# Kernel tuning notes

Hardware: AMD Instinct MI355X
Metric: run time of the kernel (lower is better)

Reference implementation:

```python
import jax, jax.numpy as jnp
import numpy as np

S, H, T = 65536, 768, 6   # seq_len, hidden, n_types
K, WIN = 3, 15            # top-k starts, end-pointer window
TYPE_THRESH, START_THRESH = 0.3, 0.15


def setup_inputs() -> dict:
    key = jax.random.key(0)
    ks = jax.random.split(key, 9)
    sc = 0.02
    return {
        "token_embeds": jax.random.normal(ks[0], (S, H), dtype=jnp.float32),
        "W_start": jax.random.normal(ks[1], (H, T), dtype=jnp.float32) * sc,
        "b_start": jnp.zeros((T,), dtype=jnp.float32),
        "W_end": jax.random.normal(ks[2], (H, T), dtype=jnp.float32) * sc,
        "b_end": jnp.zeros((T,), dtype=jnp.float32),
        "W1": jax.random.normal(ks[3], (H, 64), dtype=jnp.float32) * sc,
        "b1": jnp.zeros((64,), dtype=jnp.float32),
        "W2": jax.random.normal(ks[4], (64, T), dtype=jnp.float32) * sc,
        "b2": jnp.zeros((T,), dtype=jnp.float32),
    }


def reference(token_embeds, W_start, b_start, W_end, b_end, W1, b1, W2, b2):
    # Pointer projections: (S, T)
    start_scores = token_embeds @ W_start + b_start
    end_scores = token_embeds @ W_end + b_end

    # Type confidence head on mean-pooled embedding (torch nn.GELU = exact erf)
    pooled = token_embeds.mean(axis=0)                      # (H,)
    h = jax.nn.gelu(pooled @ W1 + b1, approximate=False)    # (64,)
    type_conf = jax.nn.sigmoid(h @ W2 + b2)                 # (T,)

    # Softmax over sequence dim per type, then top-3 candidate starts per type
    s_probs = jax.nn.softmax(start_scores, axis=0)          # (S, T)
    top_vals, top_idx = jax.lax.top_k(s_probs.T, K)         # (T, K)

    # Windowed argmax over end_scores[s : s+15, t]
    pos = top_idx[:, :, None] + jnp.arange(WIN)
    in_range = pos < S
    pos_c = jnp.clip(pos, 0, S - 1)
    end_T = end_scores.T                                    # (T, S)
    window_vals = end_T[jnp.arange(T)[:, None, None], pos_c]
    window_vals = jnp.where(in_range, window_vals, -jnp.inf)
    e_off = jnp.argmax(window_vals, axis=-1)                # (T, K)

    starts = top_idx                                        # (T, K) int
    ends = top_idx + e_off + 1                              # exclusive end, matches e+1
    valid = (type_conf[:, None] >= TYPE_THRESH) & (top_vals >= START_THRESH)
    conf = jnp.where(valid, top_vals * type_conf[:, None], 0.0)  # (T, K)

    return conf, starts, ends, valid
```

## Files before the change

### kernel.cpp

```cpp
#include <hip/hip_runtime.h>
#include <math.h>

#define S_TOK 65536
#define H_DIM 768
#define T_TYPES 6
#define K_TOP 3
#define WIN 15
#define NBLK1 512
#define NWAVES (NBLK1 * 4)
#define ROWS_PER_WAVE (S_TOK / NWAVES)
#define POOL_CHUNKS 8
#define BLK_PER_CHUNK (NBLK1 / POOL_CHUNKS)

__device__ __forceinline__ void top3_insert(float v, int i,
    float& v0, float& v1, float& v2, int& i0, int& i1, int& i2)
{
    if (v > v0 || (v == v0 && i < i0)) {
        v2 = v1; i2 = i1; v1 = v0; i1 = i0; v0 = v; i0 = i;
    } else if (v > v1 || (v == v1 && i < i1)) {
        v2 = v1; i2 = i1; v1 = v; i1 = i;
    } else if (v > v2 || (v == v2 && i < i2)) {
        v2 = v; i2 = i;
    }
}

__device__ __forceinline__ void merge_state(
    float& M, float& se, float& v0, float& v1, float& v2,
    int& i0, int& i1, int& i2,
    float Mb, float seb, float w0, float w1, float w2,
    int j0, int j1, int j2)
{
    const float Mn = fmaxf(M, Mb);
    se = se * expf(M - Mn) + seb * expf(Mb - Mn);
    M = Mn;
    top3_insert(w0, j0, v0, v1, v2, i0, i1, i2);
    top3_insert(w1, j1, v0, v1, v2, i0, i1, i2);
    top3_insert(w2, j2, v0, v1, v2, i0, i1, i2);
}

__global__ __launch_bounds__(256, 2) void k_scores(
    const float* __restrict__ emb,
    const float* __restrict__ Wstart, const float* __restrict__ bstart,
    const float* __restrict__ Wend,   const float* __restrict__ bend,
    float* __restrict__ endS,
    float* __restrict__ partials,
    float* __restrict__ pooledPart)
{
    const int lane = threadIdx.x & 63;
    const int wib  = threadIdx.x >> 6;
    const int wave = blockIdx.x * 4 + wib;

    const bool b5 = (lane & 32) != 0;
    const bool b4 = (lane & 16) != 0;
    const bool b3 = (lane & 8)  != 0;
    const bool b2 = (lane & 4)  != 0;
    const int  sem = (b5 ? 6 : 0) + (b4 ? 3 : 0) + (b3 ? 2 : (b2 ? 1 : 0));
    const bool desig   = ((lane & 3) == 0) && !(b3 && b2);
    const bool isStart = desig && !b5;
    const bool isEnd   = desig && b5;

    float wS[3][4][T_TYPES], wE[3][4][T_TYPES];
#pragma unroll
    for (int j = 0; j < 3; ++j)
#pragma unroll
        for (int c = 0; c < 4; ++c) {
            const int h = 4 * (lane + 64 * j) + c;
#pragma unroll
            for (int t = 0; t < T_TYPES; ++t) {
                wS[j][c][t] = Wstart[h * T_TYPES + t];
                wE[j][c][t] = Wend  [h * T_TYPES + t];
            }
        }

    float myBias = 0.0f;
    if (isStart) myBias = bstart[sem];
    if (isEnd)   myBias = bend[sem - T_TYPES];

    float pool[3][4] = {};

    float M  = -3.402823466e38f, se = 0.0f;
    float v0 = -3.402823466e38f, v1 = v0, v2 = v0;
    int   i0 = -1, i1 = -1, i2 = -1;

    const int r0 = wave * ROWS_PER_WAVE;
    const float4* rowp = (const float4*)emb + (size_t)r0 * (H_DIM / 4);
    float4 c0 = rowp[lane], c1 = rowp[lane + 64], c2 = rowp[lane + 128];

    for (int r = r0; r < r0 + ROWS_PER_WAVE; ++r) {
        const float4* nextp = rowp + ((r + 1 < S_TOK) ? (H_DIM / 4) : 0);
        float4 n0 = nextp[lane], n1 = nextp[lane + 64], n2 = nextp[lane + 128];

        float acc[12];
#pragma unroll
        for (int a = 0; a < 12; ++a) acc[a] = 0.0f;

        const float4 ee[3] = {c0, c1, c2};
#pragma unroll
        for (int j = 0; j < 3; ++j) {
            const float ev[4] = {ee[j].x, ee[j].y, ee[j].z, ee[j].w};
#pragma unroll
            for (int c = 0; c < 4; ++c) {
                const float v = ev[c];
                pool[j][c] += v;
#pragma unroll
                for (int t = 0; t < T_TYPES; ++t) {
                    acc[t]           = fmaf(v, wS[j][c][t], acc[t]);
                    acc[T_TYPES + t] = fmaf(v, wE[j][c][t], acc[T_TYPES + t]);
                }
            }
        }

        float na[6];
#pragma unroll
        for (int t = 0; t < 6; ++t) {
            const float snd  = b5 ? acc[t] : acc[t + 6];
            const float keep = b5 ? acc[t + 6] : acc[t];
            na[t] = keep + __shfl_xor(snd, 32, 64);
        }
        float nb[3];
#pragma unroll
        for (int t = 0; t < 3; ++t) {
            const float snd  = b4 ? na[t] : na[t + 3];
            const float keep = b4 ? na[t + 3] : na[t];
            nb[t] = keep + __shfl_xor(snd, 16, 64);
        }
        float nc0, nc1;
        {
            const float snd  = b3 ? nb[2] : nb[0];
            const float keep = b3 ? nb[2] : nb[0];
            nc0 = keep + __shfl_xor(b3 ? nb[0] : nb[2], 8, 64);
            (void)snd;
            nc1 = nb[1] + __shfl_xor(nb[1], 8, 64);
        }
        float d;
        {
            const float snd  = (b3 || b2) ? nc0 : nc1;
            const float keep = (!b3 && b2) ? nc1 : nc0;
            d = keep + __shfl_xor(snd, 4, 64);
        }
        d += __shfl_xor(d, 2, 64);
        d += __shfl_xor(d, 1, 64);

        const float v = d + myBias;

        if (isStart) {
            if (v > M) {
                se = se * expf(M - v) + 1.0f;
                v2 = v1; i2 = i1; v1 = v0; i1 = i0; v0 = v; i0 = r;
                M = v;
            } else {
                se += expf(v - M);
                if (v > v2 || (v == v2 && r < i2)) {
                    if (v > v1 || (v == v1 && r < i1)) {
                        v2 = v1; i2 = i1; v1 = v; i1 = r;
                    } else { v2 = v; i2 = r; }
                }
            }
        } else if (isEnd) {
            endS[(size_t)(sem - T_TYPES) * S_TOK + r] = v;
        }

        c0 = n0; c1 = n1; c2 = n2; rowp = nextp;
    }

    if (isStart) {
        float* p = partials + ((size_t)wave * T_TYPES + sem) * 8;
        p[0] = M;  p[1] = se; p[2] = v0; p[3] = v1; p[4] = v2;
        p[5] = __int_as_float(i0);
        p[6] = __int_as_float(i1);
        p[7] = __int_as_float(i2);
    }

    __shared__ float lds[4][H_DIM];
#pragma unroll
    for (int j = 0; j < 3; ++j) {
        float4 pv = make_float4(pool[j][0], pool[j][1], pool[j][2], pool[j][3]);
        ((float4*)lds[wib])[lane + 64 * j] = pv;
    }
    __syncthreads();
    for (int h = threadIdx.x; h < H_DIM; h += 256) {
        pooledPart[(size_t)blockIdx.x * H_DIM + h] =
            (lds[0][h] + lds[1][h]) + (lds[2][h] + lds[3][h]);
    }
}

__global__ __launch_bounds__(1024) void k_mid(
    const float* __restrict__ partials,
    const float* __restrict__ pooledPart,
    const float* __restrict__ W1,
    float* __restrict__ zpart,
    float* __restrict__ res)
{
    const int b = blockIdx.x;
    const int tid = threadIdx.x;

    if (b >= T_TYPES) {
        const int c = b - T_TYPES;
        __shared__ float pl[H_DIM];
        if (tid < H_DIM) {
            const float* base = pooledPart + (size_t)c * BLK_PER_CHUNK * H_DIM + tid;
            float s0 = 0, s1 = 0, s2 = 0, s3 = 0;
            for (int i = 0; i < BLK_PER_CHUNK; i += 4) {
                s0 += base[(size_t)(i + 0) * H_DIM];
                s1 += base[(size_t)(i + 1) * H_DIM];
                s2 += base[(size_t)(i + 2) * H_DIM];
                s3 += base[(size_t)(i + 3) * H_DIM];
            }
            pl[tid] = (s0 + s1) + (s2 + s3);
        }
        __syncthreads();
        const int o = tid & 63, seg = tid >> 6;
        float z = 0.0f;
        const int h0 = seg * 48;
        for (int i = 0; i < 48; ++i)
            z = fmaf(pl[h0 + i], W1[(size_t)(h0 + i) * 64 + o], z);
        __shared__ float zred[16][64];
        zred[seg][o] = z;
        __syncthreads();
        if (tid < 64) {
            float s = 0.0f;
#pragma unroll
            for (int g = 0; g < 16; ++g) s += zred[g][tid];
            zpart[c * 64 + tid] = s;
        }
        return;
    }

    float M, se, v0, v1, v2; int i0, i1, i2;
    {
        const float* p = partials + ((size_t)tid * T_TYPES + b) * 8;
        M = p[0]; se = p[1]; v0 = p[2]; v1 = p[3]; v2 = p[4];
        i0 = __float_as_int(p[5]); i1 = __float_as_int(p[6]); i2 = __float_as_int(p[7]);
    }
    {
        const float* p = partials + ((size_t)(tid + 1024) * T_TYPES + b) * 8;
        merge_state(M, se, v0, v1, v2, i0, i1, i2,
                    p[0], p[1], p[2], p[3], p[4],
                    __float_as_int(p[5]), __float_as_int(p[6]), __float_as_int(p[7]));
    }

#pragma unroll
    for (int msk = 1; msk < 64; msk <<= 1) {
        const float Mb  = __shfl_xor(M,  msk, 64);
        const float seb = __shfl_xor(se, msk, 64);
        const float w0  = __shfl_xor(v0, msk, 64);
        const float w1  = __shfl_xor(v1, msk, 64);
        const float w2  = __shfl_xor(v2, msk, 64);
        const int   j0  = __shfl_xor(i0, msk, 64);
        const int   j1  = __shfl_xor(i1, msk, 64);
        const int   j2  = __shfl_xor(i2, msk, 64);
        merge_state(M, se, v0, v1, v2, i0, i1, i2, Mb, seb, w0, w1, w2, j0, j1, j2);
    }

    __shared__ float sm[16][8];
    if ((tid & 63) == 0) {
        const int w = tid >> 6;
        sm[w][0] = M;  sm[w][1] = se;
        sm[w][2] = v0; sm[w][3] = v1; sm[w][4] = v2;
        sm[w][5] = __int_as_float(i0);
        sm[w][6] = __int_as_float(i1);
        sm[w][7] = __int_as_float(i2);
    }
    __syncthreads();
    if (tid == 0) {
        for (int w = 1; w < 16; ++w) {
            merge_state(M, se, v0, v1, v2, i0, i1, i2,
                        sm[w][0], sm[w][1], sm[w][2], sm[w][3], sm[w][4],
                        __float_as_int(sm[w][5]), __float_as_int(sm[w][6]),
                        __float_as_int(sm[w][7]));
        }
        float* r = res + b * 8;
        r[0] = v0; r[1] = v1; r[2] = v2;
        r[3] = __int_as_float(i0);
        r[4] = __int_as_float(i1);
        r[5] = __int_as_float(i2);
        r[6] = M; r[7] = se;
    }
}

__global__ __launch_bounds__(256) void k_final(
    const float* __restrict__ zpart,
    const float* __restrict__ b1,
    const float* __restrict__ W2, const float* __restrict__ b2,
    const float* __restrict__ endS, const float* __restrict__ res,
    float* __restrict__ out)
{
    const int tid = threadIdx.x;
    __shared__ float hdn[64];
    if (tid < 64) {
        float zs = 0.0f;
#pragma unroll
        for (int c = 0; c < POOL_CHUNKS; ++c) zs += zpart[c * 64 + tid];
        const float z = zs * (1.0f / (float)S_TOK) + b1[tid];
        hdn[tid] = 0.5f * z * (1.0f + erff(z * 0.7071067811865475f));
    }
    __syncthreads();

    __shared__ float tconf[T_TYPES];
    if (tid < T_TYPES) {
        float z = b2[tid];
        for (int i = 0; i < 64; ++i) z = fmaf(hdn[i], W2[i * T_TYPES + tid], z);
        tconf[tid] = 1.0f / (1.0f + expf(-z));
    }
    __syncthreads();

    if (tid < T_TYPES * K_TOP) {
        const int t = tid / K_TOP;
        const int k = tid % K_TOP;
        const float* r = res + t * 8;
        const float vraw = r[k];
        const int   idx  = __float_as_int(r[3 + k]);
        const float M    = r[6];
        const float SE   = r[7];
        const float prob = expf(vraw - M) / SE;

        const float* ecol = endS + (size_t)t * S_TOK;
        float best = -3.402823466e38f;
        int   boff = 0;
#pragma unroll
        for (int w = 0; w < WIN; ++w) {
            const int pos = idx + w;
            if (pos < S_TOK) {
                const float ev = ecol[pos];
                if (ev > best) { best = ev; boff = w; }
            }
        }
        const float tc = tconf[t];
        const bool valid = (tc >= 0.3f) && (prob >= 0.15f);
        out[tid]      = valid ? prob * tc : 0.0f;
        out[18 + tid] = (float)idx;
        out[36 + tid] = (float)(idx + boff + 1);
        out[54 + tid] = valid ? 1.0f : 0.0f;
    }
}

extern "C" void kernel_launch(void* const* d_in, const int* in_sizes, int n_in,
                              void* d_out, int out_size, void* d_ws, size_t ws_size,
                              hipStream_t stream)
{
    const float* emb    = (const float*)d_in[0];
    const float* Wstart = (const float*)d_in[1];
    const float* bstart = (const float*)d_in[2];
    const float* Wend   = (const float*)d_in[3];
    const float* bend   = (const float*)d_in[4];
    const float* W1     = (const float*)d_in[5];
    const float* b1     = (const float*)d_in[6];
    const float* W2     = (const float*)d_in[7];
    const float* b2     = (const float*)d_in[8];
    float* out = (float*)d_out;

    float* ws       = (float*)d_ws;
    float* endS     = ws;
    float* partials = endS + (size_t)T_TYPES * S_TOK;
    float* pp       = partials + (size_t)NWAVES * T_TYPES * 8;
    float* zpart    = pp + (size_t)NBLK1 * H_DIM;
    float* res      = zpart + (size_t)POOL_CHUNKS * 64;

    k_scores<<<NBLK1, 256, 0, stream>>>(emb, Wstart, bstart, Wend, bend,
                                        endS, partials, pp);
    k_mid<<<T_TYPES + POOL_CHUNKS, 1024, 0, stream>>>(partials, pp, W1, zpart, res);
    k_final<<<1, 256, 0, stream>>>(zpart, b1, W2, b2, endS, res, out);
}
```

Baseline: 341.0 us.

## Split projection types across waves sharing rows to cut register pressure

Each block now owns a contiguous row range, and its four waves all read the same rows. Each wave computes three output columns: start or end, types 0-2 or 3-5. This cuts per-lane weight registers from 144 to 36 and simplifies the cross-lane shuffle reduction, which allows a higher occupancy bound of 4 blocks per CU and 2048 blocks. The cost is that each row is loaded by four waves, so the design relies on L1/L2 to absorb the redundant reads, and the number of pooled and start partials to merge downstream grows.

After: 349.3 us. 2.5% more time.

```diff
diff --git a/kernel.cpp b/kernel.cpp
--- a/kernel.cpp
+++ b/kernel.cpp
@@ -6,10 +6,10 @@
 #define T_TYPES 6
 #define K_TOP 3
 #define WIN 15
-#define NBLK1 512
-#define NWAVES (NBLK1 * 4)
-#define ROWS_PER_WAVE (S_TOK / NWAVES)
-#define POOL_CHUNKS 8
+#define NBLK1 2048
+#define ROWS_PER_BLK (S_TOK / NBLK1)
+#define NRANGES NBLK1
+#define POOL_CHUNKS 16
 #define BLK_PER_CHUNK (NBLK1 / POOL_CHUNKS)
 
 __device__ __forceinline__ void top3_insert(float v, int i,
@@ -38,7 +38,7 @@
     top3_insert(w2, j2, v0, v1, v2, i0, i1, i2);
 }
 
-__global__ __launch_bounds__(256, 2) void k_scores(
+__global__ __launch_bounds__(256, 4) void k_scores(
     const float* __restrict__ emb,
     const float* __restrict__ Wstart, const float* __restrict__ bstart,
     const float* __restrict__ Wend,   const float* __restrict__ bend,
@@ -48,139 +48,109 @@
 {
     const int lane = threadIdx.x & 63;
     const int wib  = threadIdx.x >> 6;
-    const int wave = blockIdx.x * 4 + wib;
-
+    const bool isStartW = (wib < 2);
+    const int  tbase = (wib & 1) * 3;
     const bool b5 = (lane & 32) != 0;
     const bool b4 = (lane & 16) != 0;
-    const bool b3 = (lane & 8)  != 0;
-    const bool b2 = (lane & 4)  != 0;
-    const int  sem = (b5 ? 6 : 0) + (b4 ? 3 : 0) + (b3 ? 2 : (b2 ? 1 : 0));
-    const bool desig   = ((lane & 3) == 0) && !(b3 && b2);
-    const bool isStart = desig && !b5;
-    const bool isEnd   = desig && b5;
-
-    float wS[3][4][T_TYPES], wE[3][4][T_TYPES];
+    const int  sem = b4 ? 2 : (b5 ? 1 : 0);
+    const bool desig = (lane == 0) || (lane == 16) || (lane == 32);
+
+    const float* Wmat = isStartW ? Wstart : Wend;
+    float wG[3][4][3];
 #pragma unroll
     for (int j = 0; j < 3; ++j)
 #pragma unroll
         for (int c = 0; c < 4; ++c) {
             const int h = 4 * (lane + 64 * j) + c;
 #pragma unroll
-            for (int t = 0; t < T_TYPES; ++t) {
-                wS[j][c][t] = Wstart[h * T_TYPES + t];
-                wE[j][c][t] = Wend  [h * T_TYPES + t];
-            }
+            for (int u = 0; u < 3; ++u)
+                wG[j][c][u] = Wmat[h * T_TYPES + tbase + u];
         }
 
     float myBias = 0.0f;
-    if (isStart) myBias = bstart[sem];
-    if (isEnd)   myBias = bend[sem - T_TYPES];
-
-    float pool[3][4] = {};
+    if (desig) myBias = (isStartW ? bstart : bend)[tbase + sem];
+
+    float4 pool[3];
+#pragma unroll
+    for (int j = 0; j < 3; ++j) pool[j] = make_float4(0.f, 0.f, 0.f, 0.f);
 
     float M  = -3.402823466e38f, se = 0.0f;
     float v0 = -3.402823466e38f, v1 = v0, v2 = v0;
     int   i0 = -1, i1 = -1, i2 = -1;
 
-    const int r0 = wave * ROWS_PER_WAVE;
+    const int r0 = blockIdx.x * ROWS_PER_BLK;
     const float4* rowp = (const float4*)emb + (size_t)r0 * (H_DIM / 4);
     float4 c0 = rowp[lane], c1 = rowp[lane + 64], c2 = rowp[lane + 128];
 
-    for (int r = r0; r < r0 + ROWS_PER_WAVE; ++r) {
+    for (int r = r0; r < r0 + ROWS_PER_BLK; ++r) {
         const float4* nextp = rowp + ((r + 1 < S_TOK) ? (H_DIM / 4) : 0);
         float4 n0 = nextp[lane], n1 = nextp[lane + 64], n2 = nextp[lane + 128];
 
-        float acc[12];
-#pragma unroll
-        for (int a = 0; a < 12; ++a) acc[a] = 0.0f;
-
+        float a0 = 0.0f, a1 = 0.0f, a2 = 0.0f;
         const float4 ee[3] = {c0, c1, c2};
 #pragma unroll
         for (int j = 0; j < 3; ++j) {
             const float ev[4] = {ee[j].x, ee[j].y, ee[j].z, ee[j].w};
+            pool[j].x += ev[0]; pool[j].y += ev[1];
+            pool[j].z += ev[2]; pool[j].w += ev[3];
 #pragma unroll
             for (int c = 0; c < 4; ++c) {
                 const float v = ev[c];
-                pool[j][c] += v;
-#pragma unroll
-                for (int t = 0; t < T_TYPES; ++t) {
-                    acc[t]           = fmaf(v, wS[j][c][t], acc[t]);
-                    acc[T_TYPES + t] = fmaf(v, wE[j][c][t], acc[T_TYPES + t]);
+                a0 = fmaf(v, wG[j][c][0], a0);
+                a1 = fmaf(v, wG[j][c][1], a1);
+                a2 = fmaf(v, wG[j][c][2], a2);
+            }
+        }
+
+        float snd = b5 ? a0 : a1;
+        float kp  = b5 ? a1 : a0;
+        float x0 = kp + __shfl_xor(snd, 32, 64);
+        float x1 = a2 + __shfl_xor(a2, 32, 64);
+        snd = b4 ? x0 : x1;
+        kp  = b4 ? x1 : x0;
+        float y = kp + __shfl_xor(snd, 16, 64);
+        y += __shfl_xor(y, 8, 64);
+        y += __shfl_xor(y, 4, 64);
+        y += __shfl_xor(y, 2, 64);
+        y += __shfl_xor(y, 1, 64);
+
+        const float v = y + myBias;
+
+        if (isStartW) {
+            if (desig) {
+                if (v > M) {
+                    se = se * expf(M - v) + 1.0f;
+                    v2 = v1; i2 = i1; v1 = v0; i1 = i0; v0 = v; i0 = r;
+                    M = v;
+                } else {
+                    se += expf(v - M);
+                    if (v > v2 || (v == v2 && r < i2)) {
+                        if (v > v1 || (v == v1 && r < i1)) {
+                            v2 = v1; i2 = i1; v1 = v; i1 = r;
+                        } else { v2 = v; i2 = r; }
+                    }
                 }
             }
-        }
-
-        float na[6];
-#pragma unroll
-        for (int t = 0; t < 6; ++t) {
-            const float snd  = b5 ? acc[t] : acc[t + 6];
-            const float keep = b5 ? acc[t + 6] : acc[t];
-            na[t] = keep + __shfl_xor(snd, 32, 64);
-        }
-        float nb[3];
-#pragma unroll
-        for (int t = 0; t < 3; ++t) {
-            const float snd  = b4 ? na[t] : na[t + 3];
-            const float keep = b4 ? na[t + 3] : na[t];
-            nb[t] = keep + __shfl_xor(snd, 16, 64);
-        }
-        float nc0, nc1;
-        {
-            const float snd  = b3 ? nb[2] : nb[0];
-            const float keep = b3 ? nb[2] : nb[0];
-            nc0 = keep + __shfl_xor(b3 ? nb[0] : nb[2], 8, 64);
-            (void)snd;
-            nc1 = nb[1] + __shfl_xor(nb[1], 8, 64);
-        }
-        float d;
-        {
-            const float snd  = (b3 || b2) ? nc0 : nc1;
-            const float keep = (!b3 && b2) ? nc1 : nc0;
-            d = keep + __shfl_xor(snd, 4, 64);
-        }
-        d += __shfl_xor(d, 2, 64);
-        d += __shfl_xor(d, 1, 64);
-
-        const float v = d + myBias;
-
-        if (isStart) {
-            if (v > M) {
-                se = se * expf(M - v) + 1.0f;
-                v2 = v1; i2 = i1; v1 = v0; i1 = i0; v0 = v; i0 = r;
-                M = v;
-            } else {
-                se += expf(v - M);
-                if (v > v2 || (v == v2 && r < i2)) {
-                    if (v > v1 || (v == v1 && r < i1)) {
-                        v2 = v1; i2 = i1; v1 = v; i1 = r;
-                    } else { v2 = v; i2 = r; }
-                }
-            }
-        } else if (isEnd) {
-            endS[(size_t)(sem - T_TYPES) * S_TOK + r] = v;
+        } else {
+            if (desig) endS[(size_t)(tbase + sem) * S_TOK + r] = v;
         }
 
         c0 = n0; c1 = n1; c2 = n2; rowp = nextp;
     }
 
-    if (isStart) {
-        float* p = partials + ((size_t)wave * T_TYPES + sem) * 8;
+    if (isStartW && desig) {
+        float* p = partials + ((size_t)blockIdx.x * T_TYPES + (tbase + sem)) * 8;
         p[0] = M;  p[1] = se; p[2] = v0; p[3] = v1; p[4] = v2;
         p[5] = __int_as_float(i0);
         p[6] = __int_as_float(i1);
         p[7] = __int_as_float(i2);
     }
 
-    __shared__ float lds[4][H_DIM];
-#pragma unroll
-    for (int j = 0; j < 3; ++j) {
-        float4 pv = make_float4(pool[j][0], pool[j][1], pool[j][2], pool[j][3]);
-        ((float4*)lds[wib])[lane + 64 * j] = pv;
-    }
-    __syncthreads();
-    for (int h = threadIdx.x; h < H_DIM; h += 256) {
-        pooledPart[(size_t)blockIdx.x * H_DIM + h] =
-            (lds[0][h] + lds[1][h]) + (lds[2][h] + lds[3][h]);
+    if (wib == 3) {
+        float4* pp4 = (float4*)(pooledPart + (size_t)blockIdx.x * H_DIM);
+        pp4[lane]       = pool[0];
+        pp4[lane + 64]  = pool[1];
+        pp4[lane + 128] = pool[2];
     }
 }
 
@@ -199,14 +169,14 @@
         __shared__ float pl[H_DIM];
         if (tid < H_DIM) {
             const float* base = pooledPart + (size_t)c * BLK_PER_CHUNK * H_DIM + tid;
-            float s0 = 0, s1 = 0, s2 = 0, s3 = 0;
-            for (int i = 0; i < BLK_PER_CHUNK; i += 4) {
-                s0 += base[(size_t)(i + 0) * H_DIM];
-                s1 += base[(size_t)(i + 1) * H_DIM];
-                s2 += base[(size_t)(i + 2) * H_DIM];
-                s3 += base[(size_t)(i + 3) * H_DIM];
+            float s[8] = {0, 0, 0, 0, 0, 0, 0, 0};
+            for (int i = 0; i < BLK_PER_CHUNK; i += 8) {
+#pragma unroll
+                for (int u = 0; u < 8; ++u)
+                    s[u] += base[(size_t)(i + u) * H_DIM];
             }
-            pl[tid] = (s0 + s1) + (s2 + s3);
+            pl[tid] = ((s[0] + s[1]) + (s[2] + s[3])) +
+                      ((s[4] + s[5]) + (s[6] + s[7]));
         }
         __syncthreads();
         const int o = tid & 63, seg = tid >> 6;
@@ -352,7 +322,7 @@
     float* ws       = (float*)d_ws;
     float* endS     = ws;
     float* partials = endS + (size_t)T_TYPES * S_TOK;
-    float* pp       = partials + (size_t)NWAVES * T_TYPES * 8;
+    float* pp       = partials + (size_t)NRANGES * T_TYPES * 8;
     float* zpart    = pp + (size_t)NBLK1 * H_DIM;
     float* res      = zpart + (size_t)POOL_CHUNKS * 64;
 
```

## Fuse final kernel into mid via last-block ticket; write per-wave pooled partials

Applied to the files above, without the earlier changes.

Removes the third kernel launch by having the last block of k_mid, chosen with an atomic ticket, compute the type-confidence head and the windowed end argmax. k_scores now writes per-wave pooled partials straight to global memory instead of reducing the four waves through LDS with a block barrier. POOL_CHUNKS is doubled so more blocks share the larger pooled reduction. The cost is a fourfold larger pooled-partial buffer to read back, plus atomic stores and fences to make the cross-block handoff safe.

Measured after the change: 350.8 us. +2.9%, slower.

```diff
diff --git a/kernel.cpp b/kernel.cpp
--- a/kernel.cpp
+++ b/kernel.cpp
@@ -9,8 +9,9 @@
 #define NBLK1 512
 #define NWAVES (NBLK1 * 4)
 #define ROWS_PER_WAVE (S_TOK / NWAVES)
-#define POOL_CHUNKS 8
-#define BLK_PER_CHUNK (NBLK1 / POOL_CHUNKS)
+#define POOL_CHUNKS 16
+#define BLK_PER_CHUNK (NWAVES / POOL_CHUNKS)
+#define NBLK2 (T_TYPES + POOL_CHUNKS)
 
 __device__ __forceinline__ void top3_insert(float v, int i,
     float& v0, float& v1, float& v2, int& i0, int& i1, int& i2)
@@ -44,8 +45,11 @@
     const float* __restrict__ Wend,   const float* __restrict__ bend,
     float* __restrict__ endS,
     float* __restrict__ partials,
-    float* __restrict__ pooledPart)
-{
+    float* __restrict__ pooledPart,
+    int* __restrict__ ticket)
+{
+    if (blockIdx.x == 0 && threadIdx.x == 0) *ticket = 0;
+
     const int lane = threadIdx.x & 63;
     const int wib  = threadIdx.x >> 6;
     const int wave = blockIdx.x * 4 + wib;
@@ -126,10 +130,8 @@
         }
         float nc0, nc1;
         {
-            const float snd  = b3 ? nb[2] : nb[0];
             const float keep = b3 ? nb[2] : nb[0];
             nc0 = keep + __shfl_xor(b3 ? nb[0] : nb[2], 8, 64);
-            (void)snd;
             nc1 = nb[1] + __shfl_xor(nb[1], 8, 64);
         }
         float d;
@@ -171,42 +173,45 @@
         p[7] = __int_as_float(i2);
     }
 
-    __shared__ float lds[4][H_DIM];
-#pragma unroll
-    for (int j = 0; j < 3; ++j) {
-        float4 pv = make_float4(pool[j][0], pool[j][1], pool[j][2], pool[j][3]);
-        ((float4*)lds[wib])[lane + 64 * j] = pv;
-    }
-    __syncthreads();
-    for (int h = threadIdx.x; h < H_DIM; h += 256) {
-        pooledPart[(size_t)blockIdx.x * H_DIM + h] =
-            (lds[0][h] + lds[1][h]) + (lds[2][h] + lds[3][h]);
-    }
+    float4* pp4 = (float4*)(pooledPart + (size_t)wave * H_DIM);
+    pp4[lane]       = make_float4(pool[0][0], pool[0][1], pool[0][2], pool[0][3]);
+    pp4[lane + 64]  = make_float4(pool[1][0], pool[1][1], pool[1][2], pool[1][3]);
+    pp4[lane + 128] = make_float4(pool[2][0], pool[2][1], pool[2][2], pool[2][3]);
 }
 
 __global__ __launch_bounds__(1024) void k_mid(
     const float* __restrict__ partials,
     const float* __restrict__ pooledPart,
-    const float* __restrict__ W1,
+    const float* __restrict__ W1, const float* __restrict__ b1,
+    const float* __restrict__ W2, const float* __restrict__ b2,
+    const float* __restrict__ endS,
     float* __restrict__ zpart,
-    float* __restrict__ res)
+    float* __restrict__ res,
+    int* __restrict__ ticket,
+    float* __restrict__ out)
 {
     const int b = blockIdx.x;
     const int tid = threadIdx.x;
 
+    __shared__ float pl[H_DIM];
+    __shared__ float zred[16][64];
+    __shared__ float sm[16][8];
+    __shared__ float hdn[64];
+    __shared__ float tconf[T_TYPES];
+    __shared__ int sLast;
+
     if (b >= T_TYPES) {
         const int c = b - T_TYPES;
-        __shared__ float pl[H_DIM];
         if (tid < H_DIM) {
             const float* base = pooledPart + (size_t)c * BLK_PER_CHUNK * H_DIM + tid;
-            float s0 = 0, s1 = 0, s2 = 0, s3 = 0;
-            for (int i = 0; i < BLK_PER_CHUNK; i += 4) {
-                s0 += base[(size_t)(i + 0) * H_DIM];
-                s1 += base[(size_t)(i + 1) * H_DIM];
-                s2 += base[(size_t)(i + 2) * H_DIM];
-                s3 += base[(size_t)(i + 3) * H_DIM];
-            }
-            pl[tid] = (s0 + s1) + (s2 + s3);
+            float s[8] = {0, 0, 0, 0, 0, 0, 0, 0};
+            for (int i = 0; i < BLK_PER_CHUNK; i += 8) {
+#pragma unroll
+                for (int u = 0; u < 8; ++u)
+                    s[u] += base[(size_t)(i + u) * H_DIM];
+            }
+            pl[tid] = ((s[0] + s[1]) + (s[2] + s[3])) +
+                      ((s[4] + s[5]) + (s[6] + s[7]));
         }
         __syncthreads();
         const int o = tid & 63, seg = tid >> 6;
@@ -214,89 +219,93 @@
         const int h0 = seg * 48;
         for (int i = 0; i < 48; ++i)
             z = fmaf(pl[h0 + i], W1[(size_t)(h0 + i) * 64 + o], z);
-        __shared__ float zred[16][64];
         zred[seg][o] = z;
         __syncthreads();
         if (tid < 64) {
             float s = 0.0f;
 #pragma unroll
             for (int g = 0; g < 16; ++g) s += zred[g][tid];
-            zpart[c * 64 + tid] = s;
-        }
-        return;
-    }
-
-    float M, se, v0, v1, v2; int i0, i1, i2;
-    {
-        const float* p = partials + ((size_t)tid * T_TYPES + b) * 8;
-        M = p[0]; se = p[1]; v0 = p[2]; v1 = p[3]; v2 = p[4];
-        i0 = __float_as_int(p[5]); i1 = __float_as_int(p[6]); i2 = __float_as_int(p[7]);
-    }
-    {
-        const float* p = partials + ((size_t)(tid + 1024) * T_TYPES + b) * 8;
-        merge_state(M, se, v0, v1, v2, i0, i1, i2,
-                    p[0], p[1], p[2], p[3], p[4],
-                    __float_as_int(p[5]), __float_as_int(p[6]), __float_as_int(p[7]));
-    }
-
-#pragma unroll
-    for (int msk = 1; msk < 64; msk <<= 1) {
-        const float Mb  = __shfl_xor(M,  msk, 64);
-        const float seb = __shfl_xor(se, msk, 64);
-        const float w0  = __shfl_xor(v0, msk, 64);
-        const float w1  = __shfl_xor(v1, msk, 64);
-        const float w2  = __shfl_xor(v2, msk, 64);
-        const int   j0  = __shfl_xor(i0, msk, 64);
-        const int   j1  = __shfl_xor(i1, msk, 64);
-        const int   j2  = __shfl_xor(i2, msk, 64);
-        merge_state(M, se, v0, v1, v2, i0, i1, i2, Mb, seb, w0, w1, w2, j0, j1, j2);
-    }
-
-    __shared__ float sm[16][8];
-    if ((tid & 63) == 0) {
-        const int w = tid >> 6;
-        sm[w][0] = M;  sm[w][1] = se;
-        sm[w][2] = v0; sm[w][3] = v1; sm[w][4] = v2;
-        sm[w][5] = __int_as_float(i0);
-        sm[w][6] = __int_as_float(i1);
-        sm[w][7] = __int_as_float(i2);
-    }
+            __hip_atomic_store(&zpart[c * 64 + tid], s,
+                               __ATOMIC_RELAXED, __HIP_MEMORY_SCOPE_AGENT);
+        }
+    } else {
+        float M, se, v0, v1, v2; int i0, i1, i2;
+        {
+            const float* p = partials + ((size_t)tid * T_TYPES + b) * 8;
+            M = p[0]; se = p[1]; v0 = p[2]; v1 = p[3]; v2 = p[4];
+            i0 = __float_as_int(p[5]); i1 = __float_as_int(p[6]);
+            i2 = __float_as_int(p[7]);
+        }
+        {
+            const float* p = partials + ((size_t)(tid + 1024) * T_TYPES + b) * 8;
+            merge_state(M, se, v0, v1, v2, i0, i1, i2,
+                        p[0], p[1], p[2], p[3], p[4],
+                        __float_as_int(p[5]), __float_as_int(p[6]),
+                        __float_as_int(p[7]));
+        }
+#pragma unroll
+        for (int msk = 1; msk < 64; msk <<= 1) {
+            const float Mb  = __shfl_xor(M,  msk, 64);
+            const float seb = __shfl_xor(se, msk, 64);
+            const float w0  = __shfl_xor(v0, msk, 64);
+            const float w1  = __shfl_xor(v1, msk, 64);
+            const float w2  = __shfl_xor(v2, msk, 64);
+            const int   j0  = __shfl_xor(i0, msk, 64);
+            const int   j1  = __shfl_xor(i1, msk, 64);
+            const int   j2  = __shfl_xor(i2, msk, 64);
+            merge_state(M, se, v0, v1, v2, i0, i1, i2, Mb, seb, w0, w1, w2,
+                        j0, j1, j2);
+        }
+        if ((tid & 63) == 0) {
+            const int w = tid >> 6;
+            sm[w][0] = M;  sm[w][1] = se;
+            sm[w][2] = v0; sm[w][3] = v1; sm[w][4] = v2;
+            sm[w][5] = __int_as_float(i0);
+            sm[w][6] = __int_as_float(i1);
+            sm[w][7] = __int_as_float(i2);
+        }
+        __syncthreads();
+        if (tid == 0) {
+            for (int w = 1; w < 16; ++w) {
+                merge_state(M, se, v0, v1, v2, i0, i1, i2,
+                            sm[w][0], sm[w][1], sm[w][2], sm[w][3], sm[w][4],
+                            __float_as_int(sm[w][5]), __float_as_int(sm[w][6]),
+                            __float_as_int(sm[w][7]));
+            }
+            float* r = res + b * 8;
+            __hip_atomic_store(&r[0], v0, __ATOMIC_RELAXED, __HIP_MEMORY_SCOPE_AGENT);
+            __hip_atomic_store(&r[1], v1, __ATOMIC_RELAXED, __HIP_MEMORY_SCOPE_AGENT);
+            __hip_atomic_store(&r[2], v2, __ATOMIC_RELAXED, __HIP_MEMORY_SCOPE_AGENT);
+            __hip_atomic_store(&r[3], __int_as_float(i0), __ATOMIC_RELAXED, __HIP_MEMORY_SCOPE_AGENT);
+            __hip_atomic_store(&r[4], __int_as_float(i1), __ATOMIC_RELAXED, __HIP_MEMORY_SCOPE_AGENT);
+            __hip_atomic_store(&r[5], __int_as_float(i2), __ATOMIC_RELAXED, __HIP_MEMORY_SCOPE_AGENT);
+            __hip_atomic_store(&r[6], M,  __ATOMIC_RELAXED, __HIP_MEMORY_SCOPE_AGENT);
+            __hip_atomic_store(&r[7], se, __ATOMIC_RELAXED, __HIP_MEMORY_SCOPE_AGENT);
+        }
+    }
+
+    __threadfence();
     __syncthreads();
     if (tid == 0) {
-        for (int w = 1; w < 16; ++w) {
-            merge_state(M, se, v0, v1, v2, i0, i1, i2,
-                        sm[w][0], sm[w][1], sm[w][2], sm[w][3], sm[w][4],
-                        __float_as_int(sm[w][5]), __float_as_int(sm[w][6]),
-                        __float_as_int(sm[w][7]));
-        }
-        float* r = res + b * 8;
-        r[0] = v0; r[1] = v1; r[2] = v2;
-        r[3] = __int_as_float(i0);
-        r[4] = __int_as_float(i1);
-        r[5] = __int_as_float(i2);
-        r[6] = M; r[7] = se;
-    }
-}
-
-__global__ __launch_bounds__(256) void k_final(
-    const float* __restrict__ zpart,
-    const float* __restrict__ b1,
-    const float* __restrict__ W2, const float* __restrict__ b2,
-    const float* __restrict__ endS, const float* __restrict__ res,
-    float* __restrict__ out)
-{
-    const int tid = threadIdx.x;
-    __shared__ float hdn[64];
+        const int old = __hip_atomic_fetch_add(ticket, 1, __ATOMIC_ACQ_REL,
+                                               __HIP_MEMORY_SCOPE_AGENT);
+        sLast = (old == NBLK2 - 1);
+    }
+    __syncthreads();
+    if (!sLast) return;
+    __threadfence();
+
     if (tid < 64) {
         float zs = 0.0f;
 #pragma unroll
-        for (int c = 0; c < POOL_CHUNKS; ++c) zs += zpart[c * 64 + tid];
+        for (int c = 0; c < POOL_CHUNKS; ++c)
+            zs += __hip_atomic_load(&zpart[c * 64 + tid],
+                                    __ATOMIC_RELAXED, __HIP_MEMORY_SCOPE_AGENT);
         const float z = zs * (1.0f / (float)S_TOK) + b1[tid];
         hdn[tid] = 0.5f * z * (1.0f + erff(z * 0.7071067811865475f));
     }
     __syncthreads();
 
-    __shared__ float tconf[T_TYPES];
     if (tid < T_TYPES) {
         float z = b2[tid];
         for (int i = 0; i < 64; ++i) z = fmaf(hdn[i], W2[i * T_TYPES + tid], z);
@@ -307,11 +316,14 @@
     if (tid < T_TYPES * K_TOP) {
         const int t = tid / K_TOP;
         const int k = tid % K_TOP;
-        const float* r = res + t * 8;
-        const float vraw = r[k];
-        const int   idx  = __float_as_int(r[3 + k]);
-        const float M    = r[6];
-        const float SE   = r[7];
+        const float vraw = __hip_atomic_load(&res[t * 8 + k],
+                                __ATOMIC_RELAXED, __HIP_MEMORY_SCOPE_AGENT);
+        const int idx = __float_as_int(__hip_atomic_load(&res[t * 8 + 3 + k],
+                                __ATOMIC_RELAXED, __HIP_MEMORY_SCOPE_AGENT));
+        const float M  = __hip_atomic_load(&res[t * 8 + 6],
+                                __ATOMIC_RELAXED, __HIP_MEMORY_SCOPE_AGENT);
+        const float SE = __hip_atomic_load(&res[t * 8 + 7],
+                                __ATOMIC_RELAXED, __HIP_MEMORY_SCOPE_AGENT);
         const float prob = expf(vraw - M) / SE;
 
         const float* ecol = endS + (size_t)t * S_TOK;
@@ -353,11 +365,12 @@
     float* endS     = ws;
     float* partials = endS + (size_t)T_TYPES * S_TOK;
     float* pp       = partials + (size_t)NWAVES * T_TYPES * 8;
-    float* zpart    = pp + (size_t)NBLK1 * H_DIM;
+    float* zpart    = pp + (size_t)NWAVES * H_DIM;
     float* res      = zpart + (size_t)POOL_CHUNKS * 64;
+    int*   ticket   = (int*)(res + T_TYPES * 8);
 
     k_scores<<<NBLK1, 256, 0, stream>>>(emb, Wstart, bstart, Wend, bend,
-                                        endS, partials, pp);
-    k_mid<<<T_TYPES + POOL_CHUNKS, 1024, 0, stream>>>(partials, pp, W1, zpart, res);
-    k_final<<<1, 256, 0, stream>>>(zpart, b1, W2, b2, endS, res, out);
-}
+                                        endS, partials, pp, ticket);
+    k_mid<<<NBLK2, 1024, 0, stream>>>(partials, pp, W1, b1, W2, b2,
+                                      endS, zpart, res, ticket, out);
+}
```
